# Kernel tuning notes

Measured on AMD Instinct MI355X. Metric: run time of the kernel, lower is better.

The kernel has to match this reference:

```python
import jax, jax.numpy as jnp
import numpy as np

N_NODES = 50000
N_EDGES = 600000
ATOM_DIM = 75
HID = 128
N_LAYERS = 4
OUT_DIM = 1
NUM_GRAPHS = 128
EPS = 1e-5


def _bn(x, gamma, beta):
    # BatchNorm1d training-mode forward (biased variance)
    mu = jnp.mean(x, axis=0)
    var = jnp.mean((x - mu) ** 2, axis=0)
    return (x - mu) * jax.lax.rsqrt(var + EPS) * gamma + beta


def setup_inputs() -> dict:
    key = jax.random.key(0)
    ks = jax.random.split(key, 24)
    s = 0.05
    inp = {
        'node_features': jax.random.normal(ks[0], (N_NODES, ATOM_DIM), jnp.float32),
        'edge_index': jax.random.randint(ks[1], (2, N_EDGES), 0, N_NODES, jnp.int32),
        'batch_idx': jnp.sort(jax.random.randint(ks[2], (N_NODES,), 0, NUM_GRAPHS, jnp.int32)),
        # atom embedding: Linear(75->128) + ReLU + BN
        'emb_W': jax.random.normal(ks[3], (HID, ATOM_DIM), jnp.float32) * s,
        'emb_b': jnp.zeros((HID,), jnp.float32),
        'emb_g': jnp.ones((HID,), jnp.float32),
        'emb_beta': jnp.zeros((HID,), jnp.float32),
        # per-layer params, stacked over L=4
        'msg_W': jax.random.normal(ks[4], (N_LAYERS, HID, HID), jnp.float32) * s,
        'msg_b': jnp.zeros((N_LAYERS, HID), jnp.float32),
        'att_W': jax.random.normal(ks[5], (N_LAYERS, 2 * HID), jnp.float32) * s,
        'att_b': jnp.zeros((N_LAYERS,), jnp.float32),
        'gru_Wih': jax.random.normal(ks[6], (N_LAYERS, 3 * HID, HID), jnp.float32) * s,
        'gru_bih': jnp.zeros((N_LAYERS, 3 * HID), jnp.float32),
        'gru_Whh': jax.random.normal(ks[7], (N_LAYERS, 3 * HID, HID), jnp.float32) * s,
        'gru_bhh': jnp.zeros((N_LAYERS, 3 * HID), jnp.float32),
        'bn_g': jnp.ones((N_LAYERS, HID), jnp.float32),
        'bn_b': jnp.zeros((N_LAYERS, HID), jnp.float32),
        # readout: Linear(128->64) + ReLU + Linear(64->1)
        'ro_W1': jax.random.normal(ks[8], (HID // 2, HID), jnp.float32) * s,
        'ro_b1': jnp.zeros((HID // 2,), jnp.float32),
        'ro_W2': jax.random.normal(ks[9], (OUT_DIM, HID // 2), jnp.float32) * s,
        'ro_b2': jnp.zeros((OUT_DIM,), jnp.float32),
    }
    return inp


def _forward(node_features, edge_index, batch_idx, emb_W, emb_b, emb_g, emb_beta,
             msg_W, msg_b, att_W, att_b, gru_Wih, gru_bih, gru_Whh, gru_bhh,
             bn_g, bn_b, ro_W1, ro_b1, ro_W2, ro_b2):
    src, dst = edge_index[0], edge_index[1]
    # atom embedding
    x = _bn(jax.nn.relu(node_features @ emb_W.T + emb_b), emb_g, emb_beta)
    for l in range(N_LAYERS):
        xs = x[src]                                   # [E, h] gather
        xd = x[dst]                                   # [E, h] gather
        ef = jnp.concatenate([xs, xd], axis=1)        # [E, 2h]
        att = jax.nn.sigmoid(ef @ att_W[l] + att_b[l])  # [E]
        msgs = (xs @ msg_W[l].T + msg_b[l]) * att[:, None]  # [E, h]
        agg = jax.ops.segment_sum(msgs, dst, num_segments=N_NODES)  # [N, h]
        # GRUCell(agg, x)
        gi = agg @ gru_Wih[l].T + gru_bih[l]
        gh = x @ gru_Whh[l].T + gru_bhh[l]
        i_r, i_z, i_n = jnp.split(gi, 3, axis=1)
        h_r, h_z, h_n = jnp.split(gh, 3, axis=1)
        r = jax.nn.sigmoid(i_r + h_r)
        z = jax.nn.sigmoid(i_z + h_z)
        n = jnp.tanh(i_n + r * h_n)
        h_new = (1.0 - z) * n + z * x
        x = _bn(h_new, bn_g[l], bn_b[l])              # dropout is identity in eval
    # graph readout: sum-pool per graph
    graph_repr = jax.ops.segment_sum(x, batch_idx, num_segments=NUM_GRAPHS)  # [G, h]
    h1 = jax.nn.relu(graph_repr @ ro_W1.T + ro_b1)
    return h1 @ ro_W2.T + ro_b2                       # [G, 1]


def reference(node_features, edge_index, batch_idx, emb_W, emb_b, emb_g, emb_beta,
              msg_W, msg_b, att_W, att_b, gru_Wih, gru_bih, gru_Whh, gru_bhh,
              bn_g, bn_b, ro_W1, ro_b1, ro_W2, ro_b2):
    return _forward(node_features, edge_index, batch_idx, emb_W, emb_b, emb_g, emb_beta,
                    msg_W, msg_b, att_W, att_b, gru_Wih, gru_bih, gru_Whh, gru_bhh,
                    bn_g, bn_b, ro_W1, ro_b1, ro_W2, ro_b2)
```

## Files before the change

kernel.cpp:

```cpp
#include <hip/hip_runtime.h>
#include <math.h>

#define NN 50000
#define NE 600000
#define ADIM 75
#define HID 128
#define NLAYERS 4
#define NGRAPHS 128
#define BN_EPS 1e-5f
#define NNP 50048
#define NB128 (NNP / 128)

typedef short bhalf8 __attribute__((ext_vector_type(8)));
typedef float floatx4 __attribute__((ext_vector_type(4)));

__device__ __forceinline__ float sigm(float v) { return 1.0f / (1.0f + __expf(-v)); }
__device__ __forceinline__ float tanh_f(float v) {
    return 1.0f - 2.0f / (__expf(2.0f * v) + 1.0f);
}

__device__ __forceinline__ unsigned short f2bf(float f) {
    unsigned u = __builtin_bit_cast(unsigned, f);
    u = (u + 0x7FFFu + ((u >> 16) & 1u)) >> 16;
    return (unsigned short)u;
}
__device__ __forceinline__ float bf2f(unsigned short h) {
    return __builtin_bit_cast(float, ((unsigned)h) << 16);
}

__device__ __forceinline__ void gl2lds16(const void* g, void* l) {
    __builtin_amdgcn_global_load_lds(
        (const __attribute__((address_space(1))) unsigned int*)g,
        (__attribute__((address_space(3))) unsigned int*)l, 16, 0, 0);
}

__global__ __launch_bounds__(256) void k_nfb(
    const float* __restrict__ nf, unsigned short* __restrict__ nfb)
{
    int e = blockIdx.x * 256 + threadIdx.x;
    if (e >= NN * 24) return;
    int n = e / 24, k4 = e - n * 24;
    ushort4 o;
    int k = k4 * 4;
    o.x = (k + 0 < ADIM) ? f2bf(nf[(size_t)n * ADIM + k + 0]) : 0;
    o.y = (k + 1 < ADIM) ? f2bf(nf[(size_t)n * ADIM + k + 1]) : 0;
    o.z = (k + 2 < ADIM) ? f2bf(nf[(size_t)n * ADIM + k + 2]) : 0;
    o.w = (k + 3 < ADIM) ? f2bf(nf[(size_t)n * ADIM + k + 3]) : 0;
    ((ushort4*)nfb)[(size_t)n * 24 + k4] = o;
}

__global__ __launch_bounds__(256) void k_wfrag_emb(
    const float* __restrict__ W, unsigned short* __restrict__ web)
{
    int e = blockIdx.x * 256 + threadIdx.x;
    int j = e & 7, n = (e >> 3) & 15, quad = (e >> 7) & 3;
    int kb = (e >> 9) % 3, tc = e / 1536;
    int row = tc * 16 + n;
    int kk = kb * 32 + quad * 8 + j;
    web[e] = (kk < ADIM) ? f2bf(W[row * ADIM + kk]) : 0;
}

__global__ __launch_bounds__(512) void k_embed_m(
    const unsigned short* __restrict__ nfb, const unsigned short* __restrict__ web,
    const float* __restrict__ b, float* __restrict__ y,
    float* __restrict__ bnsum)
{
    __shared__ __align__(16) unsigned short wbe[12288];
    __shared__ float sred[1024], sred2[1024];
    const int t = threadIdx.x;
    const int wave = t >> 6, lane = t & 63;
    const int col = lane & 15, quad = (lane >> 4) & 3;
    const int node0 = blockIdx.x * 128;

    {
        const char* gsrc = (const char*)web + wave * 3072 + lane * 16;
        char* ldst = (char*)wbe + wave * 3072;
#pragma unroll
        for (int i = 0; i < 3; i++)
            gl2lds16(gsrc + i * 1024, ldst + i * 1024);
    }

    const int anode = node0 + wave * 16 + col;
    bhalf8 afN[3];
#pragma unroll
    for (int kb = 0; kb < 3; kb++)
        afN[kb] = *(const bhalf8*)&nfb[(size_t)anode * 96 + kb * 32 + quad * 8];

    floatx4 acc[8];
#pragma unroll
    for (int tc = 0; tc < 8; tc++) {
        float bv = b[tc * 16 + col];
        acc[tc] = (floatx4){bv, bv, bv, bv};
    }
    __syncthreads();

#pragma unroll
    for (int tc = 0; tc < 8; tc++) {
        bhalf8 bfr[3];
#pragma unroll
        for (int kb = 0; kb < 3; kb++)
            bfr[kb] = *(const bhalf8*)&wbe[((tc * 3 + kb) * 64 + lane) * 8];
#pragma unroll
        for (int kb = 0; kb < 3; kb++)
            acc[tc] = __builtin_amdgcn_mfma_f32_16x16x32_bf16(afN[kb], bfr[kb], acc[tc], 0, 0, 0);
    }

    float ps[8], ps2[8];
#pragma unroll
    for (int tc = 0; tc < 8; tc++) {
        ps[tc] = 0.f; ps2[tc] = 0.f;
#pragma unroll
        for (int e = 0; e < 4; e++) {
            float v = fmaxf(acc[tc][e], 0.0f);
            int nd = node0 + wave * 16 + quad * 4 + e;
            if (nd < NN) {
                y[(size_t)nd * HID + tc * 16 + col] = v;
                ps[tc] += v; ps2[tc] += v * v;
            }
        }
    }
#pragma unroll
    for (int tc = 0; tc < 8; tc++) {
        ps[tc]  += __shfl_xor(ps[tc], 16);  ps2[tc] += __shfl_xor(ps2[tc], 16);
        ps[tc]  += __shfl_xor(ps[tc], 32);  ps2[tc] += __shfl_xor(ps2[tc], 32);
    }
    if (quad == 0) {
#pragma unroll
        for (int tc = 0; tc < 8; tc++) {
            sred[wave * 128 + tc * 16 + col]  = ps[tc];
            sred2[wave * 128 + tc * 16 + col] = ps2[tc];
        }
    }
    __syncthreads();
    if (t < 128) {
        float s = 0.f, s2 = 0.f;
#pragma unroll
        for (int w = 0; w < 8; w++) { s += sred[w * 128 + t]; s2 += sred2[w * 128 + t]; }
        unsafeAtomicAdd(&bnsum[t], s);
        unsafeAtomicAdd(&bnsum[128 + t], s2);
    }
}

__global__ __launch_bounds__(256) void k_bnx(
    const float* __restrict__ y, const float* __restrict__ bnsum,
    const float* __restrict__ g, const float* __restrict__ beta,
    const float* __restrict__ attW,
    unsigned short* __restrict__ xb,
    float* __restrict__ as_, float* __restrict__ ad_)
{
    const int t = threadIdx.x;
    const int n = blockIdx.x * 4 + (t >> 6);
    const int lane = t & 63;
    const int f0 = lane * 2;
    float m0 = bnsum[f0] * (1.0f / NN);
    float v0 = bnsum[128 + f0] * (1.0f / NN) - m0 * m0;
    float m1 = bnsum[f0 + 1] * (1.0f / NN);
    float v1 = bnsum[128 + f0 + 1] * (1.0f / NN) - m1 * m1;
    float sc0 = g[f0] * rsqrtf(v0 + BN_EPS);
    float sc1 = g[f0 + 1] * rsqrtf(v1 + BN_EPS);
    float sh0 = beta[f0] - m0 * sc0;
    float sh1 = beta[f0 + 1] - m1 * sc1;

    float2 v = ((const float2*)y)[(size_t)n * 64 + lane];
    float2 xv;
    xv.x = v.x * sc0 + sh0;
    xv.y = v.y * sc1 + sh1;
    unsigned pk = (unsigned)f2bf(xv.x) | ((unsigned)f2bf(xv.y) << 16);
    ((unsigned*)xb)[(size_t)n * 64 + lane] = pk;
    float2 aws = ((const float2*)attW)[lane];
    float2 awd = ((const float2*)(attW + 128))[lane];
    float pas = xv.x * aws.x + xv.y * aws.y;
    float pad = xv.x * awd.x + xv.y * awd.y;
#pragma unroll
    for (int msk = 32; msk >= 1; msk >>= 1) {
        pas += __shfl_xor(pas, msk);
        pad += __shfl_xor(pad, msk);
    }
    if (lane == 0) { as_[n] = pas; ad_[n] = pad; }
}

__global__ __launch_bounds__(128) void k_wc(
    const float* __restrict__ Wih, const float* __restrict__ Wm,
    const float* __restrict__ bm, float* __restrict__ Wc, float* __restrict__ bmih)
{
    __shared__ float sw[128];
    __shared__ float red[128];
    const int b = blockIdx.x;
    const int l = b / 384, r = b - l * 384;
    const int t = threadIdx.x;
    const float* wihrow = Wih + ((size_t)l * 384 + r) * 128;
    sw[t] = wihrow[t];
    __syncthreads();
    const float* wm = Wm + (size_t)l * 128 * 128;
    float acc = 0.f;
#pragma unroll 8
    for (int k = 0; k < 128; k++) acc += sw[k] * wm[k * 128 + t];
    Wc[((size_t)l * 384 + r) * 128 + t] = acc;
    red[t] = sw[t] * bm[l * 128 + t];
    __syncthreads();
#pragma unroll
    for (int off = 64; off >= 1; off >>= 1) {
        if (t < off) red[t] += red[t + off];
        __syncthreads();
    }
    if (t == 0) bmih[l * 384 + r] = red[0];
}

__global__ __launch_bounds__(256) void k_frag(
    const float* __restrict__ Wc, const float* __restrict__ Whh,
    unsigned short* __restrict__ wcb, unsigned short* __restrict__ whhb)
{
    const int b = blockIdx.x;
    const int mat = b / 192;
    const int e = (b - mat * 192) * 256 + threadIdx.x;
    const int l = mat >> 1, which = mat & 1;
    const float* src = which ? (Whh + (size_t)l * 49152) : (Wc + (size_t)l * 49152);
    unsigned short* dst = which ? (whhb + (size_t)l * 49152) : (wcb + (size_t)l * 49152);
    int j = e & 7, n = (e >> 3) & 15, quad = (e >> 7) & 3;
    int kb = (e >> 9) & 3, tc = (e >> 11) & 7, g = (e >> 14) & 3;
    int row = g * 128 + tc * 16 + n;
    int kk = kb * 32 + quad * 8 + j;
    dst[e] = f2bf(src[row * 128 + kk]);
}

__global__ __launch_bounds__(256) void k_count(const int* __restrict__ dst, int* __restrict__ cnt)
{
    int e = blockIdx.x * 256 + threadIdx.x;
    if (e < NE) atomicAdd(&cnt[dst[e]], 1);
}

#define SCAN_B 512
#define SCAN_G 98

__global__ __launch_bounds__(SCAN_B) void k_scan1(
    const int* __restrict__ cnt, int* __restrict__ rowptr, int* __restrict__ bsum)
{
    __shared__ int s[SCAN_B];
    const int t = threadIdx.x;
    const int i = blockIdx.x * SCAN_B + t;
    int v = (i < NN) ? cnt[i] : 0;
    s[t] = v;
    __syncthreads();
#pragma unroll
    for (int off = 1; off < SCAN_B; off <<= 1) {
        int u = (t >= off) ? s[t - off] : 0;
        __syncthreads();
        s[t] += u;
        __syncthreads();
    }
    if (i < NN) rowptr[i] = s[t] - v;
    if (t == SCAN_B - 1) bsum[blockIdx.x] = s[t];
}

__global__ __launch_bounds__(128) void k_scan2(int* __restrict__ bsum, int* __restrict__ rowptr)
{
    __shared__ int s[128];
    const int t = threadIdx.x;
    int v = (t < SCAN_G) ? bsum[t] : 0;
    s[t] = v;
    __syncthreads();
#pragma unroll
    for (int off = 1; off < 128; off <<= 1) {
        int u = (t >= off) ? s[t - off] : 0;
        __syncthreads();
        s[t] += u;
        __syncthreads();
    }
    if (t < SCAN_G) bsum[t] = s[t] - v;
    if (t == 127) rowptr[NN] = s[127];
}

__global__ __launch_bounds__(SCAN_B) void k_scan3(
    int* __restrict__ rowptr, const int* __restrict__ bsum, int* __restrict__ wptr)
{
    const int i = blockIdx.x * SCAN_B + threadIdx.x;
    if (i < NN) {
        int v = rowptr[i] + bsum[blockIdx.x];
        rowptr[i] = v;
        wptr[i] = v;
    }
}

__global__ __launch_bounds__(256) void k_scatter(
    const int* __restrict__ src, const int* __restrict__ dst,
    int* __restrict__ wptr, int* __restrict__ ssrc)
{
    int e = blockIdx.x * 256 + threadIdx.x;
    if (e < NE) {
        int d = dst[e];
        int pos = atomicAdd(&wptr[d], 1);
        ssrc[pos] = src[e];
    }
}

__global__ __launch_bounds__(256) void k_gather(
    const int* __restrict__ rowptr, const int* __restrict__ ssrc,
    const unsigned short* __restrict__ xb, const float* __restrict__ as_,
    const float* __restrict__ ad_, const float* __restrict__ attb, int l,
    unsigned short* __restrict__ aggxb, float* __restrict__ sumatt)
{
    const int t = threadIdx.x;
    const int n = blockIdx.x * 8 + (t >> 5);
    const int lane = t & 31;
    const int r0 = rowptr[n], r1 = rowptr[n + 1];
    const float adv = ad_[n] + attb[l];
    float4 acc = make_float4(0.f, 0.f, 0.f, 0.f);
    float satt = 0.f;

    int ids[8], ids2[8];
    if (r0 < r1) {
#pragma unroll
        for (int k = 0; k < 8; k++) {
            int idx = r0 + k; if (idx >= r1) idx = r1 - 1;
            ids[k] = ssrc[idx];
        }
    }
    for (int base = r0; base < r1; base += 8) {
        const int nxt = base + 8;
        if (nxt < r1) {
#pragma unroll
            for (int k = 0; k < 8; k++) {
                int idx = nxt + k; if (idx >= r1) idx = r1 - 1;
                ids2[k] = ssrc[idx];
            }
        }
        ushort4 v[8];
        float a[8];
#pragma unroll
        for (int k = 0; k < 8; k++) {
            v[k] = ((const ushort4*)xb)[(size_t)ids[k] * 32 + lane];
            a[k] = as_[ids[k]];
        }
#pragma unroll
        for (int k = 0; k < 8; k++) {
            if (base + k < r1) {
                float att = sigm(a[k] + adv);
                acc.x += bf2f(v[k].x) * att; acc.y += bf2f(v[k].y) * att;
                acc.z += bf2f(v[k].z) * att; acc.w += bf2f(v[k].w) * att;
                satt += att;
            }
        }
#pragma unroll
        for (int k = 0; k < 8; k++) ids[k] = ids2[k];
    }
    ushort4 o;
    o.x = f2bf(acc.x); o.y = f2bf(acc.y); o.z = f2bf(acc.z); o.w = f2bf(acc.w);
    ((ushort4*)aggxb)[(size_t)n * 32 + lane] = o;
    if (lane == 0) sumatt[n] = satt;
}

#define STAGE_W(SRC)                                                          \
    {                                                                         \
        const char* gsrc = (const char*)(SRC) + wave * 4096 + lane * 16;      \
        char* ldst = (char*)wbuf + wave * 4096;                               \
        _Pragma("unroll")                                                     \
        for (int i = 0; i < 4; i++)                                           \
            gl2lds16(gsrc + i * 1024, ldst + i * 1024);                       \
    }

#define MMGL(AF, ACC)                                                         \
    _Pragma("unroll")                                                         \
    for (int tc = 0; tc < 8; tc++) {                                          \
        bhalf8 bfr[4];                                                        \
        _Pragma("unroll")                                                     \
        for (int kb = 0; kb < 4; kb++)                                        \
            bfr[kb] = *(const bhalf8*)&wbuf[((tc * 4 + kb) * 64 + lane) * 8]; \
        _Pragma("unroll")                                                     \
        for (int kb = 0; kb < 4; kb++)                                        \
            ACC[tc] = __builtin_amdgcn_mfma_f32_16x16x32_bf16(AF[kb], bfr[kb], ACC[tc], 0, 0, 0); \
    }

__global__ __launch_bounds__(512) void k_gru(
    const unsigned short* __restrict__ aggxb, const float* __restrict__ sumatt,
    const unsigned short* __restrict__ xb,
    const unsigned short* __restrict__ wcb, const float* __restrict__ bmih,
    const float* __restrict__ bih,
    const unsigned short* __restrict__ whhb, const float* __restrict__ bhh,
    float* __restrict__ y, float* __restrict__ bnsum)
{
    __shared__ __align__(16) unsigned short wbuf[16384];
    __shared__ float sred[1024], sred2[1024];
    const int t = threadIdx.x;
    const int wave = t >> 6, lane = t & 63;
    const int col = lane & 15, quad = (lane >> 4) & 3;
    const int node0 = blockIdx.x * 128;

    STAGE_W(wcb + 0 * 16384);

    const int anode = node0 + wave * 16 + col;
    bhalf8 afA[4], afX[4];
#pragma unroll
    for (int kb = 0; kb < 4; kb++) {
        afA[kb] = *(const bhalf8*)&aggxb[(size_t)anode * HID + kb * 32 + quad * 8];
        afX[kb] = *(const bhalf8*)&xb[(size_t)anode * HID + kb * 32 + quad * 8];
    }
    float sa[4];
#pragma unroll
    for (int e = 0; e < 4; e++) sa[e] = sumatt[node0 + wave * 16 + quad * 4 + e];

    floatx4 accR[8], accN[8];

#pragma unroll
    for (int tc = 0; tc < 8; tc++) {
        int f = 0 * 128 + tc * 16 + col;
        float b0 = bih[f] + bhh[f], bm = bmih[f];
        accR[tc] = (floatx4){b0 + sa[0] * bm, b0 + sa[1] * bm, b0 + sa[2] * bm, b0 + sa[3] * bm};
    }
    __syncthreads();
    MMGL(afA, accR);
    __syncthreads();
    STAGE_W(whhb + 0 * 16384);
    __syncthreads();
    MMGL(afX, accR);
    __syncthreads();
    STAGE_W(whhb + 2 * 16384);
#pragma unroll
    for (int tc = 0; tc < 8; tc++)
#pragma unroll
        for (int e = 0; e < 4; e++)
            accR[tc][e] = sigm(accR[tc][e]);

#pragma unroll
    for (int tc = 0; tc < 8; tc++) {
        float bh = bhh[2 * 128 + tc * 16 + col];
        accN[tc] = (floatx4){bh, bh, bh, bh};
    }
    __syncthreads();
    MMGL(afX, accN);
    __syncthreads();
    STAGE_W(wcb + 2 * 16384);
#pragma unroll
    for (int tc = 0; tc < 8; tc++) {
        int f = 2 * 128 + tc * 16 + col;
        float bi = bih[f], bm = bmih[f];
#pragma unroll
        for (int e = 0; e < 4; e++)
            accN[tc][e] = accR[tc][e] * accN[tc][e] + bi + sa[e] * bm;
    }
    __syncthreads();
    MMGL(afA, accN);
    __syncthreads();
    STAGE_W(wcb + 1 * 16384);
#pragma unroll
    for (int tc = 0; tc < 8; tc++)
#pragma unroll
        for (int e = 0; e < 4; e++)
            accN[tc][e] = tanh_f(accN[tc][e]);

#pragma unroll
    for (int tc = 0; tc < 8; tc++) {
        int f = 1 * 128 + tc * 16 + col;
        float b0 = bih[f] + bhh[f], bm = bmih[f];
        accR[tc] = (floatx4){b0 + sa[0] * bm, b0 + sa[1] * bm, b0 + sa[2] * bm, b0 + sa[3] * bm};
    }
    __syncthreads();
    MMGL(afA, accR);
    __syncthreads();
    STAGE_W(whhb + 1 * 16384);
    __syncthreads();
    MMGL(afX, accR);

    float ps[8], ps2[8];
#pragma unroll
    for (int tc = 0; tc < 8; tc++) {
        ps[tc] = 0.f; ps2[tc] = 0.f;
#pragma unroll
        for (int e = 0; e < 4; e++) {
            float z = sigm(accR[tc][e]);
            int nd = node0 + wave * 16 + quad * 4 + e;
            float xv = bf2f(xb[(size_t)nd * HID + tc * 16 + col]);
            float h = (1.0f - z) * accN[tc][e] + z * xv;
            if (nd < NN) {
                y[(size_t)nd * HID + tc * 16 + col] = h;
                ps[tc] += h; ps2[tc] += h * h;
            }
        }
    }
#pragma unroll
    for (int tc = 0; tc < 8; tc++) {
        ps[tc]  += __shfl_xor(ps[tc], 16);  ps2[tc] += __shfl_xor(ps2[tc], 16);
        ps[tc]  += __shfl_xor(ps[tc], 32);  ps2[tc] += __shfl_xor(ps2[tc], 32);
    }
    if (quad == 0) {
#pragma unroll
        for (int tc = 0; tc < 8; tc++) {
            sred[wave * 128 + tc * 16 + col]  = ps[tc];
            sred2[wave * 128 + tc * 16 + col] = ps2[tc];
        }
    }
    __syncthreads();
    if (t < 128) {
        float s = 0.f, s2 = 0.f;
#pragma unroll
        for (int w = 0; w < 8; w++) { s += sred[w * 128 + t]; s2 += sred2[w * 128 + t]; }
        unsafeAtomicAdd(&bnsum[t], s);
        unsafeAtomicAdd(&bnsum[128 + t], s2);
    }
}

__global__ __launch_bounds__(256) void k_pool(
    const unsigned short* __restrict__ xb, const int* __restrict__ batch,
    float* __restrict__ gr)
{
    __shared__ int sb[256];
    const int t = threadIdx.x;
    const int nb = blockIdx.x * 256;
    int ld = nb + t; if (ld >= NN) ld = NN - 1;
    sb[t] = batch[ld];
    __syncthreads();
    const int s = t >> 7, f = t & 127;
    float acc = 0.f; int cur = -1;
    for (int i = s; i < 256; i += 2) {
        int n = nb + i;
        if (n >= NN) break;
        int g = sb[i];
        if (g != cur) {
            if (cur >= 0) unsafeAtomicAdd(&gr[(size_t)cur * HID + f], acc);
            acc = 0.f; cur = g;
        }
        acc += bf2f(xb[(size_t)n * HID + f]);
    }
    if (cur >= 0) unsafeAtomicAdd(&gr[(size_t)cur * HID + f], acc);
}

__global__ __launch_bounds__(64) void k_readout(
    const float* __restrict__ gr, const float* __restrict__ W1,
    const float* __restrict__ b1, const float* __restrict__ W2,
    const float* __restrict__ b2, float* __restrict__ out)
{
    const int g = blockIdx.x, j = threadIdx.x;
    float acc = b1[j];
    const float4* grow = (const float4*)&gr[g * HID];
    const float4* wrow = (const float4*)&W1[j * HID];
#pragma unroll
    for (int k4 = 0; k4 < 32; k4++) {
        float4 a = grow[k4], w = wrow[k4];
        acc += a.x * w.x + a.y * w.y + a.z * w.z + a.w * w.w;
    }
    float h = fmaxf(acc, 0.0f) * W2[j];
#pragma unroll
    for (int msk = 32; msk >= 1; msk >>= 1) h += __shfl_xor(h, msk);
    if (j == 0) out[g] = h + b2[0];
}

extern "C" void kernel_launch(void* const* d_in, const int* in_sizes, int n_in,
                              void* d_out, int out_size, void* d_ws, size_t ws_size,
                              hipStream_t stream)
{
    const float* nf    = (const float*)d_in[0];
    const int*   ei    = (const int*)d_in[1];
    const int*   batch = (const int*)d_in[2];
    const float* embW  = (const float*)d_in[3];
    const float* embb  = (const float*)d_in[4];
    const float* embg  = (const float*)d_in[5];
    const float* embbe = (const float*)d_in[6];
    const float* msgW  = (const float*)d_in[7];
    const float* msgb  = (const float*)d_in[8];
    const float* attW  = (const float*)d_in[9];
    const float* attb  = (const float*)d_in[10];
    const float* Wih   = (const float*)d_in[11];
    const float* bih   = (const float*)d_in[12];
    const float* Whh   = (const float*)d_in[13];
    const float* bhh   = (const float*)d_in[14];
    const float* bng   = (const float*)d_in[15];
    const float* bnb   = (const float*)d_in[16];
    const float* roW1  = (const float*)d_in[17];
    const float* rob1  = (const float*)d_in[18];
    const float* roW2  = (const float*)d_in[19];
    const float* rob2  = (const float*)d_in[20];
    const int* src = ei;
    const int* dst = ei + NE;
    float* out = (float*)d_out;

    char* base = (char*)d_ws;
    const size_t NH = (size_t)NN * HID;
    float* bnsum = (float*)base;
    float* y     = (float*)(base + 10240);
    unsigned short* xb    = (unsigned short*)(y + NH);
    unsigned short* aggxb = xb + NH;
    float* as_   = (float*)(aggxb + NH);
    float* ad_   = as_ + NN;
    float* sumatt= ad_ + NN;
    float* gr    = sumatt + NN;
    float* Wc    = gr + NGRAPHS * HID;
    float* bmih  = Wc + 4 * 384 * 128;
    int* rowptr  = (int*)(bmih + 4 * 384);
    int* wptr    = rowptr + NN + 4;
    int* cnt     = wptr + NN;
    int* bsum    = cnt + NN;
    int* ssrc    = bsum + 128;
    unsigned short* wcb  = (unsigned short*)(ssrc + NE);
    unsigned short* whhb = wcb + 4 * 49152;
    unsigned short* nfb  = whhb + 4 * 49152;
    unsigned short* web  = nfb + (size_t)NNP * 96;

    k_wc<<<4 * 384, 128, 0, stream>>>(Wih, msgW, msgb, Wc, bmih);
    k_frag<<<8 * 192, 256, 0, stream>>>(Wc, Whh, wcb, whhb);
    k_nfb<<<(NN * 24 + 255) / 256, 256, 0, stream>>>(nf, nfb);
    k_wfrag_emb<<<48, 256, 0, stream>>>(embW, web);
    hipMemsetAsync(cnt, 0, NN * sizeof(int), stream);
    hipMemsetAsync(bnsum, 0, 5 * 256 * sizeof(float), stream);
    k_count<<<(NE + 255) / 256, 256, 0, stream>>>(dst, cnt);
    k_scan1<<<SCAN_G, SCAN_B, 0, stream>>>(cnt, rowptr, bsum);
    k_scan2<<<1, 128, 0, stream>>>(bsum, rowptr);
    k_scan3<<<SCAN_G, SCAN_B, 0, stream>>>(rowptr, bsum, wptr);
    k_scatter<<<(NE + 255) / 256, 256, 0, stream>>>(src, dst, wptr, ssrc);

    k_embed_m<<<NB128, 512, 0, stream>>>(nfb, web, embb, y, bnsum);
    k_bnx<<<NN / 4, 256, 0, stream>>>(y, bnsum, embg, embbe, attW, xb, as_, ad_);

    for (int l = 0; l < NLAYERS; l++) {
        k_gather<<<NN / 8, 256, 0, stream>>>(rowptr, ssrc, xb, as_, ad_, attb, l, aggxb, sumatt);
        k_gru<<<NB128, 512, 0, stream>>>(
            aggxb, sumatt, xb,
            wcb + (size_t)l * 49152, bmih + (size_t)l * 384, bih + (size_t)l * 384,
            whhb + (size_t)l * 49152, bhh + (size_t)l * 384, y, bnsum + (l + 1) * 256);
        const float* attW_next = attW + (size_t)((l + 1 < NLAYERS) ? l + 1 : l) * 256;
        k_bnx<<<NN / 4, 256, 0, stream>>>(y, bnsum + (l + 1) * 256,
                                          bng + (size_t)l * HID, bnb + (size_t)l * HID,
                                          attW_next, xb, as_, ad_);
    }

    hipMemsetAsync(gr, 0, NGRAPHS * HID * sizeof(float), stream);
    k_pool<<<(NN + 255) / 256, 256, 0, stream>>>(xb, batch, gr);
    k_readout<<<NGRAPHS, 64, 0, stream>>>(gr, roW1, rob1, roW2, rob2, out);
}
```

Measured before the change: 614.4 us.

## Fuse attention gather into GRU kernel via shared-memory staging of aggregates

Removes the separate k_gather kernel and performs the per-node attention-weighted neighbor aggregation inside the GRU kernel, writing the bf16 aggregate and attention sums into shared memory instead of global buffers. This eliminates a global write/read round trip of the aggregate tensor and one launch per layer. In exchange, the gather now runs in only NB128 (~391) blocks of 512 threads, which may lower parallelism and latency hiding for the irregular gather compared with the former 6250-block launch. The workspace layout is adjusted to drop aggxb/sumatt and pad xb to NNP rows.

```diff
diff --git a/kernel.cpp b/kernel.cpp
--- a/kernel.cpp
+++ b/kernel.cpp
@@ -293,66 +293,10 @@
     }
 }
 
-__global__ __launch_bounds__(256) void k_gather(
-    const int* __restrict__ rowptr, const int* __restrict__ ssrc,
-    const unsigned short* __restrict__ xb, const float* __restrict__ as_,
-    const float* __restrict__ ad_, const float* __restrict__ attb, int l,
-    unsigned short* __restrict__ aggxb, float* __restrict__ sumatt)
-{
-    const int t = threadIdx.x;
-    const int n = blockIdx.x * 8 + (t >> 5);
-    const int lane = t & 31;
-    const int r0 = rowptr[n], r1 = rowptr[n + 1];
-    const float adv = ad_[n] + attb[l];
-    float4 acc = make_float4(0.f, 0.f, 0.f, 0.f);
-    float satt = 0.f;
-
-    int ids[8], ids2[8];
-    if (r0 < r1) {
-#pragma unroll
-        for (int k = 0; k < 8; k++) {
-            int idx = r0 + k; if (idx >= r1) idx = r1 - 1;
-            ids[k] = ssrc[idx];
-        }
-    }
-    for (int base = r0; base < r1; base += 8) {
-        const int nxt = base + 8;
-        if (nxt < r1) {
-#pragma unroll
-            for (int k = 0; k < 8; k++) {
-                int idx = nxt + k; if (idx >= r1) idx = r1 - 1;
-                ids2[k] = ssrc[idx];
-            }
-        }
-        ushort4 v[8];
-        float a[8];
-#pragma unroll
-        for (int k = 0; k < 8; k++) {
-            v[k] = ((const ushort4*)xb)[(size_t)ids[k] * 32 + lane];
-            a[k] = as_[ids[k]];
-        }
-#pragma unroll
-        for (int k = 0; k < 8; k++) {
-            if (base + k < r1) {
-                float att = sigm(a[k] + adv);
-                acc.x += bf2f(v[k].x) * att; acc.y += bf2f(v[k].y) * att;
-                acc.z += bf2f(v[k].z) * att; acc.w += bf2f(v[k].w) * att;
-                satt += att;
-            }
-        }
-#pragma unroll
-        for (int k = 0; k < 8; k++) ids[k] = ids2[k];
-    }
-    ushort4 o;
-    o.x = f2bf(acc.x); o.y = f2bf(acc.y); o.z = f2bf(acc.z); o.w = f2bf(acc.w);
-    ((ushort4*)aggxb)[(size_t)n * 32 + lane] = o;
-    if (lane == 0) sumatt[n] = satt;
-}
-
 #define STAGE_W(SRC)                                                          \
     {                                                                         \
         const char* gsrc = (const char*)(SRC) + wave * 4096 + lane * 16;      \
-        char* ldst = (char*)wbuf + wave * 4096;                               \
+        char* ldst = (char*)sbuf + wave * 4096;                               \
         _Pragma("unroll")                                                     \
         for (int i = 0; i < 4; i++)                                           \
             gl2lds16(gsrc + i * 1024, ldst + i * 1024);                       \
@@ -364,42 +308,103 @@
         bhalf8 bfr[4];                                                        \
         _Pragma("unroll")                                                     \
         for (int kb = 0; kb < 4; kb++)                                        \
-            bfr[kb] = *(const bhalf8*)&wbuf[((tc * 4 + kb) * 64 + lane) * 8]; \
+            bfr[kb] = *(const bhalf8*)&sbuf[((tc * 4 + kb) * 64 + lane) * 8]; \
         _Pragma("unroll")                                                     \
         for (int kb = 0; kb < 4; kb++)                                        \
             ACC[tc] = __builtin_amdgcn_mfma_f32_16x16x32_bf16(AF[kb], bfr[kb], ACC[tc], 0, 0, 0); \
     }
 
-__global__ __launch_bounds__(512) void k_gru(
-    const unsigned short* __restrict__ aggxb, const float* __restrict__ sumatt,
+__global__ __launch_bounds__(512) void k_ggru(
+    const int* __restrict__ rowptr, const int* __restrict__ ssrc,
+    const float* __restrict__ as_, const float* __restrict__ ad_,
+    const float* __restrict__ attb, int l,
     const unsigned short* __restrict__ xb,
     const unsigned short* __restrict__ wcb, const float* __restrict__ bmih,
     const float* __restrict__ bih,
     const unsigned short* __restrict__ whhb, const float* __restrict__ bhh,
     float* __restrict__ y, float* __restrict__ bnsum)
 {
-    __shared__ __align__(16) unsigned short wbuf[16384];
+    __shared__ __align__(16) unsigned short sbuf[16384];
     __shared__ float sred[1024], sred2[1024];
+    __shared__ float satt[128];
     const int t = threadIdx.x;
     const int wave = t >> 6, lane = t & 63;
     const int col = lane & 15, quad = (lane >> 4) & 3;
     const int node0 = blockIdx.x * 128;
 
+    {
+        const float ab = attb[l];
+        const int lane32 = t & 31;
+        const int g16 = t >> 5;
+        for (int it = 0; it < 8; ++it) {
+            const int nl = it * 16 + g16;
+            const int n = node0 + nl;
+            int r0 = 0, r1 = 0; float adv = 0.f;
+            if (n < NN) { r0 = rowptr[n]; r1 = rowptr[n + 1]; adv = ad_[n] + ab; }
+            float4 acc = make_float4(0.f, 0.f, 0.f, 0.f);
+            float sat = 0.f;
+            int ids[8], ids2[8];
+            if (r0 < r1) {
+#pragma unroll
+                for (int k = 0; k < 8; k++) {
+                    int idx = r0 + k; if (idx >= r1) idx = r1 - 1;
+                    ids[k] = ssrc[idx];
+                }
+            }
+            for (int base = r0; base < r1; base += 8) {
+                const int nxt = base + 8;
+                if (nxt < r1) {
+#pragma unroll
+                    for (int k = 0; k < 8; k++) {
+                        int idx = nxt + k; if (idx >= r1) idx = r1 - 1;
+                        ids2[k] = ssrc[idx];
+                    }
+                }
+                ushort4 v[8];
+                float a[8];
+#pragma unroll
+                for (int k = 0; k < 8; k++) {
+                    v[k] = ((const ushort4*)xb)[(size_t)ids[k] * 32 + lane32];
+                    a[k] = as_[ids[k]];
+                }
+#pragma unroll
+                for (int k = 0; k < 8; k++) {
+                    if (base + k < r1) {
+                        float att = sigm(a[k] + adv);
+                        acc.x += bf2f(v[k].x) * att; acc.y += bf2f(v[k].y) * att;
+                        acc.z += bf2f(v[k].z) * att; acc.w += bf2f(v[k].w) * att;
+                        sat += att;
+                    }
+                }
+#pragma unroll
+                for (int k = 0; k < 8; k++) ids[k] = ids2[k];
+            }
+            ushort4 o;
+            o.x = f2bf(acc.x); o.y = f2bf(acc.y); o.z = f2bf(acc.z); o.w = f2bf(acc.w);
+            *(ushort4*)((char*)sbuf + (unsigned)nl * 256u + (unsigned)lane32 * 8u) = o;
+            if (lane32 == 0) satt[nl] = sat;
+        }
+    }
+    __syncthreads();
+
+    bhalf8 afA[4], afX[4];
+    {
+        const int rloc = wave * 16 + col;
+#pragma unroll
+        for (int kb = 0; kb < 4; kb++) {
+            afA[kb] = *(const bhalf8*)((const char*)sbuf +
+                       (unsigned)rloc * 256u + (unsigned)(kb * 64 + quad * 16));
+            afX[kb] = *(const bhalf8*)&xb[(size_t)(node0 + rloc) * HID + kb * 32 + quad * 8];
+        }
+    }
+    float sa[4];
+#pragma unroll
+    for (int e = 0; e < 4; e++) sa[e] = satt[wave * 16 + quad * 4 + e];
+    __syncthreads();
+
+    floatx4 accR[8], accN[8];
+
     STAGE_W(wcb + 0 * 16384);
-
-    const int anode = node0 + wave * 16 + col;
-    bhalf8 afA[4], afX[4];
-#pragma unroll
-    for (int kb = 0; kb < 4; kb++) {
-        afA[kb] = *(const bhalf8*)&aggxb[(size_t)anode * HID + kb * 32 + quad * 8];
-        afX[kb] = *(const bhalf8*)&xb[(size_t)anode * HID + kb * 32 + quad * 8];
-    }
-    float sa[4];
-#pragma unroll
-    for (int e = 0; e < 4; e++) sa[e] = sumatt[node0 + wave * 16 + quad * 4 + e];
-
-    floatx4 accR[8], accN[8];
-
 #pragma unroll
     for (int tc = 0; tc < 8; tc++) {
         int f = 0 * 128 + tc * 16 + col;
@@ -576,12 +581,10 @@
     const size_t NH = (size_t)NN * HID;
     float* bnsum = (float*)base;
     float* y     = (float*)(base + 10240);
-    unsigned short* xb    = (unsigned short*)(y + NH);
-    unsigned short* aggxb = xb + NH;
-    float* as_   = (float*)(aggxb + NH);
+    unsigned short* xb = (unsigned short*)(y + NH);
+    float* as_   = (float*)(xb + (size_t)NNP * HID);
     float* ad_   = as_ + NN;
-    float* sumatt= ad_ + NN;
-    float* gr    = sumatt + NN;
+    float* gr    = ad_ + NN;
     float* Wc    = gr + NGRAPHS * HID;
     float* bmih  = Wc + 4 * 384 * 128;
     int* rowptr  = (int*)(bmih + 4 * 384);
@@ -610,9 +613,8 @@
     k_bnx<<<NN / 4, 256, 0, stream>>>(y, bnsum, embg, embbe, attW, xb, as_, ad_);
 
     for (int l = 0; l < NLAYERS; l++) {
-        k_gather<<<NN / 8, 256, 0, stream>>>(rowptr, ssrc, xb, as_, ad_, attb, l, aggxb, sumatt);
-        k_gru<<<NB128, 512, 0, stream>>>(
-            aggxb, sumatt, xb,
+        k_ggru<<<NB128, 512, 0, stream>>>(
+            rowptr, ssrc, as_, ad_, attb, l, xb,
             wcb + (size_t)l * 49152, bmih + (size_t)l * 384, bih + (size_t)l * 384,
             whhb + (size_t)l * 49152, bhh + (size_t)l * 384, y, bnsum + (l + 1) * 256);
         const float* attW_next = attW + (size_t)((l + 1 < NLAYERS) ? l + 1 : l) * 256;
```

Result: slower. 729.9 us (+18.8%).
